# Optimization experiments

Hardware: AMD Instinct MI355X
Metric: run time of the kernel (lower is better)

The kernel has to match this reference:

```python
import jax, jax.numpy as jnp
import numpy as np

PD = 3                      # spatial feature dim (z, y, x)
HB = 1024                   # hash base per lattice coordinate
HOFF = 512                  # offset: lattice coords assumed in [-512, 511]
FILL = np.int32(2**31 - 1)  # sentinel for padded hash slots
EPS = 2.220446049250313e-16 # np.finfo('float').eps as in the torch module

def _elev_mat():
    # Embedding onto hyperplane sum(x)=0 with std-dev scale factors
    # (canonical permutohedral-lattice elevation, Adams et al.).
    E = np.zeros((PD + 1, PD), np.float32)
    E[0] = 1.0
    for i in range(1, PD + 1):
        E[i, i - 1] = -i
        E[i, i:] = 1.0
    inv_std = np.sqrt(2.0 / 3.0) * (PD + 1)
    scale = inv_std / np.sqrt(np.arange(1, PD + 1) * np.arange(2, PD + 2))
    return (E * scale[None, :]).astype(np.float32)

_EMAT = _elev_mat()
_IU = np.triu(np.ones((PD + 1, PD + 1), bool), 1)   # j > i
_IL = np.tril(np.ones((PD + 1, PD + 1), bool), -1)  # j < i

def _hash(k):  # (..., PD) int32 -> (...,) int32, injective for |coord| < 512
    return ((k[..., 0] + HOFF) * HB + (k[..., 1] + HOFF)) * HB + (k[..., 2] + HOFF)

def permutohedral(values, features):
    """Splat-blur-slice Gaussian filter. values (N,VD), features (N,PD)."""
    N, VD = values.shape
    elevated = features @ jnp.asarray(_EMAT).T                  # (N, PD+1)
    # nearest remainder-0 lattice point (nearest multiple of PD+1, ties -> down)
    v = elevated / (PD + 1)
    up, down = jnp.ceil(v), jnp.floor(v)
    rem0 = jnp.where(up - v < v - down, up, down) * (PD + 1)
    diff = elevated - rem0
    lt = diff[:, :, None] < diff[:, None, :]
    le = diff[:, :, None] <= diff[:, None, :]
    rank = (lt & _IU).sum(-1) + (le & _IL).sum(-1)              # (N, PD+1) int32
    rank = rank + jnp.round(rem0.sum(-1) / (PD + 1)).astype(rank.dtype)[:, None]
    shift = jnp.where(rank < 0, PD + 1, 0) + jnp.where(rank > PD, -(PD + 1), 0)
    rank = rank + shift
    rem0 = rem0 + shift.astype(rem0.dtype)
    # barycentric coordinates inside the enclosing simplex
    t = (elevated - rem0) / (PD + 1)                            # (N, PD+1)
    ohA = jax.nn.one_hot(PD - rank, PD + 2, dtype=values.dtype)
    ohB = jax.nn.one_hot(PD + 1 - rank, PD + 2, dtype=values.dtype)
    b = (ohA * t[..., None]).sum(1) - (ohB * t[..., None]).sum(1)
    b = b.at[:, 0].add(1.0 + b[:, PD + 1])
    bary = b[:, :PD + 1]                                        # (N, PD+1)
    # keys of the PD+1 simplex vertices (first PD coords; last is implied)
    rem0i = rem0[:, :PD].astype(jnp.int32)
    ranki = rank[:, :PD].astype(jnp.int32)
    r = jnp.arange(PD + 1, dtype=jnp.int32)[None, :, None]
    keys = rem0i[:, None, :] + jnp.where(ranki[:, None, :] >= PD + 1 - r, r - (PD + 1), r)  # (N,PD+1,PD)
    h = _hash(keys).reshape(-1)                                 # (N*(PD+1),)
    M = h.shape[0]
    uh, inv = jnp.unique(h, size=M, fill_value=FILL, return_inverse=True)
    inv = inv.reshape(-1)
    # splat
    contrib = (values[:, None, :] * bary[:, :, None]).reshape(M, VD)
    lat = jax.ops.segment_sum(contrib, inv, num_segments=M)     # (M, VD)
    # decode unique keys from the (invertible) hash
    k2 = uh % HB - HOFF
    tq = uh // HB
    k1 = tq % HB - HOFF
    k0 = tq // HB - HOFF
    ukeys = jnp.stack([k0, k1, k2], -1).astype(jnp.int32)       # (M, PD)
    valid = (uh != FILL)[:, None]
    # blur with [0.5, 1, 0.5] along each of the PD+1 lattice directions
    def lookup(nk, lat_):
        nh = _hash(nk)
        idx = jnp.clip(jnp.searchsorted(uh, nh), 0, M - 1)
        ok = (uh[idx] == nh)[:, None]
        return jnp.where(ok, lat_[idx], 0.0)
    for j in range(PD + 1):
        o = np.ones(PD, np.int32)
        if j < PD:
            o[j] = -PD
        o = jnp.asarray(o)
        lat = jnp.where(valid, lat + 0.5 * (lookup(ukeys + o, lat) + lookup(ukeys - o, lat)), 0.0)
    # slice
    alpha = 1.0 / (1.0 + 2.0 ** (-PD))
    return alpha * jnp.einsum('nr,nrv->nv', bary, lat[inv.reshape(-1, PD + 1)])

def spatial_features(image, v_gamma, sigma_gamma):
    _, d, h, w = image.shape
    z = jnp.arange(d, dtype=jnp.float32)[:, None, None]
    y = jnp.arange(h, dtype=jnp.float32)[None, :, None]
    x = jnp.arange(w, dtype=jnp.float32)[None, None, :]
    zz = v_gamma[0] * jnp.broadcast_to(z, (d, h, w)) / sigma_gamma[0]
    xx = v_gamma[1] * jnp.broadcast_to(x, (d, h, w)) / sigma_gamma[1]
    yy = v_gamma[2] * jnp.broadcast_to(y, (d, h, w)) / sigma_gamma[2]
    return jnp.stack([zz, yy, xx], axis=3)                      # (d,h,w,3)

def setup_inputs() -> dict:
    key = jax.random.key(0)
    k1, k2 = jax.random.split(key)
    C, D, H, W = 4, 64, 128, 128
    return {
        'input_': jax.random.normal(k1, (C, D, H, W), jnp.float32),
        'image': jax.random.normal(k2, (1, D, H, W), jnp.float32),
        'v_gamma': jnp.ones((3,), jnp.float32),       # nn.Parameter init [1,1,1]
        'sigma_gamma': 5.0 * jnp.ones((3,), jnp.float32),
    }

def reference(input_, image, v_gamma, sigma_gamma):
    C, d, h, w = input_.shape
    N = d * h * w
    feats = spatial_features(image, v_gamma, sigma_gamma).reshape(N, PD)
    # filter q and the all-ones normalizer in one pass (linear per channel)
    vals = jnp.concatenate([input_.reshape(C, N).T, jnp.ones((N, 1), jnp.float32)], axis=1)
    out = permutohedral(vals, feats)
    q = out[:, :C].T.reshape(C, d, h, w)
    norm = out[:, C].reshape(1, d, h, w)
    return q * (1.0 / (norm + EPS))
```

## Files before the change

kernel.cpp:

```cpp
#include <hip/hip_runtime.h>


#define DD    64
#define HHH   128
#define WWW   128
#define NPTS  (DD * HHH * WWW)
#define LATN  (1 << 17)
#define LATF  (LATN * 5)
#define NCPY  2
#define DQ    7
#define CELLS (DQ * DQ * DQ * 4)
#define MASKW ((CELLS + 31) / 32)
#define NOID  0x7fffffff

__device__ __forceinline__ int encK(int K0, int K1, int K2) {
    return ((K2 >> 2) << 12) | ((K1 >> 2) << 7) | ((K0 >> 2) << 2) | (K0 & 3);
}

__device__ __forceinline__ int pl_geom(int z, int y, int x,
                                       const float* __restrict__ vg,
                                       const float* __restrict__ sg,
                                       int* Kout , float* bout) {
    float f0 = vg[0] * (float)z / sg[0];
    float f1 = vg[2] * (float)y / sg[2];
    float f2 = vg[1] * (float)x / sg[1];

    const float m00 = (float)2.3094010767585034;
    const float m01 = (float)1.3333333333333333;
    const float m02 = (float)0.9428090415820634;
    const float m21 = (float)-2.6666666666666665;
    const float m32 = (float)-2.8284271247461903;

    float e[4];
    e[0] =  m00 * f0 + m01 * f1 + m02 * f2;
    e[1] = -m00 * f0 + m01 * f1 + m02 * f2;
    e[2] =  m21 * f1 + m02 * f2;
    e[3] =  m32 * f2;

    float rem0[4];
    int sumr = 0;
    #pragma unroll
    for (int i = 0; i < 4; ++i) {
        rem0[i] = rintf(e[i] * 0.25f) * 4.0f;
        sumr += (int)rem0[i];
    }
    sumr /= 4;

    float diff[4];
    #pragma unroll
    for (int i = 0; i < 4; ++i) diff[i] = e[i] - rem0[i];
    int rank[4] = {0, 0, 0, 0};
    #pragma unroll
    for (int i = 0; i < 4; ++i)
        #pragma unroll
        for (int j = i + 1; j < 4; ++j) {
            if (diff[i] < diff[j]) rank[i]++; else rank[j]++;
        }

    #pragma unroll
    for (int i = 0; i < 4; ++i) {
        rank[i] += sumr;
        if (rank[i] < 0)      { rank[i] += 4; rem0[i] += 4.0f; }
        else if (rank[i] > 3) { rank[i] -= 4; rem0[i] -= 4.0f; }
    }

    float b[5] = {0.f, 0.f, 0.f, 0.f, 0.f};
    #pragma unroll
    for (int i = 0; i < 4; ++i) {
        float t = (e[i] - rem0[i]) * 0.25f;
        b[3 - rank[i]] += t;
        b[4 - rank[i]] -= t;
    }
    b[0] += 1.0f + b[4];

    int k0 = (int)rem0[0] + 16, k1 = (int)rem0[1] + 48, k2 = (int)rem0[2] + 88;
    #pragma unroll
    for (int r = 0; r < 4; ++r) {
        int o0 = (rank[0] >= 4 - r) ? (r - 4) : r;
        int o1 = (rank[1] >= 4 - r) ? (r - 4) : r;
        int o2 = (rank[2] >= 4 - r) ? (r - 4) : r;
        Kout[r * 3 + 0] = k0 + o0;
        Kout[r * 3 + 1] = k1 + o1;
        Kout[r * 3 + 2] = k2 + o2;
        bout[r] = b[r];
    }
    return ((k0 >> 2) + 32) | (((k1 >> 2) + 32) << 7) | (((k2 >> 2) + 32) << 14) |
           (rank[0] << 21) | (rank[1] << 23) | (rank[2] << 25);
}

__device__ __forceinline__ void pl_claim(int key, unsigned int* __restrict__ exists,
                                         int* __restrict__ wcnt, int* __restrict__ wl) {
    if (atomicExch(&exists[key], 1u) == 0u) {
        int p = atomicAdd(wcnt, 1);
        wl[p] = key;
    }
}

__device__ __forceinline__ int make_id(const int* K, int B0, int B1, int B2) {
    int l0 = K[0] - B0, l1 = K[1] - B1, l2 = K[2] - B2;
    if (((unsigned)l0 < 4u * DQ) & ((unsigned)l1 < 4u * DQ) & ((unsigned)l2 < 4u * DQ))
        return ((((l2 >> 2) * DQ) + (l1 >> 2)) * DQ + (l0 >> 2)) * 4 + (l0 & 3);
    return ~encK(K[0] & 127, K[1] & 127, K[2] & 127);
}

__device__ __forceinline__ void pl_emit(int id, const float* a,
                                        float* sacc, unsigned int* smask,
                                        float* __restrict__ mycopy,
                                        unsigned int* __restrict__ exists,
                                        int* __restrict__ wcnt, int* __restrict__ wl) {
    if (id >= 0) {
        #pragma unroll
        for (int c = 0; c < 5; ++c) atomicAdd(&sacc[id * 5 + c], a[c]);
        atomicOr(&smask[id >> 5], 1u << (id & 31));
    } else {
        int key = ~id;
        float* L = mycopy + (size_t)key * 5;
        #pragma unroll
        for (int c = 0; c < 5; ++c) atomicAdd(L + c, a[c]);
        pl_claim(key, exists, wcnt, wl);
    }
}

__global__ __launch_bounds__(256, 4)
void pl_splat(const float* __restrict__ vals, const float* __restrict__ vg,
              const float* __restrict__ sg, float* __restrict__ latc,
              unsigned int* __restrict__ exists,
              int* __restrict__ wcnt, int* __restrict__ wl) {
    __shared__ float4 sacc4[CELLS * 5 / 4 + 1];
    __shared__ unsigned int smask[MASKW];
    float* sacc = (float*)sacc4;
    for (int i = threadIdx.x; i < CELLS * 5 / 4 + 1; i += 256)
        sacc4[i] = make_float4(0.f, 0.f, 0.f, 0.f);
    if (threadIdx.x < MASKW) smask[threadIdx.x] = 0u;
    __syncthreads();

    int bt = blockIdx.x;
    int tx = (bt & 3) << 5;
    int ty = ((bt >> 2) & 15) << 3;
    int tz = (bt >> 6) << 2;

    float s0 = vg[0] / sg[0], s1 = vg[2] / sg[2], s2 = vg[1] / sg[1];
    const float m00 = 2.30940104f, m01 = 1.33333325f, m02 = 0.942809045f,
                m21 = -2.66666651f;
    float A0z = m00 * s0, A0y = m01 * s1, A0x = m02 * s2;
    float A1z = -A0z,     A1y = A0y,      A1x = A0x;
    float A2y = m21 * s1, A2x = A0x;
    float e0o = A0z * tz + A0y * ty + A0x * tx;
    float e1o = A1z * tz + A1y * ty + A1x * tx;
    float e2o = A2y * ty + A2x * tx;
    float e0m = e0o + fminf(0.f, A0z) * 3 + fminf(0.f, A0y) * 7 + fminf(0.f, A0x) * 31;
    float e1m = e1o + fminf(0.f, A1z) * 3 + fminf(0.f, A1y) * 7 + fminf(0.f, A1x) * 31;
    float e2m = e2o + fminf(0.f, A2y) * 7 + fminf(0.f, A2x) * 31;
    int B0 = ((int)floorf(e0m + 16.f - 7.f)) & ~3;
    int B1 = ((int)floorf(e1m + 48.f - 7.f)) & ~3;
    int B2 = ((int)floorf(e2m + 88.f - 7.f)) & ~3;

    int xs = threadIdx.x & 7;
    int xsl = ((xs & 3) << 1) | (xs >> 2);
    int x0 = tx + (xsl << 2);
    int y  = ty + ((threadIdx.x >> 3) & 7);
    int z  = tz + (threadIdx.x >> 6);
    int n0 = (z << 14) + (y << 7) + x0;

    float4 q0 = *(const float4*)(vals + n0);
    float4 q1 = *(const float4*)(vals + NPTS + n0);
    float4 q2 = *(const float4*)(vals + 2 * NPTS + n0);
    float4 q3 = *(const float4*)(vals + 3 * NPTS + n0);
    float ch0[4] = {q0.x, q0.y, q0.z, q0.w};
    float ch1[4] = {q1.x, q1.y, q1.z, q1.w};
    float ch2[4] = {q2.x, q2.y, q2.z, q2.w};
    float ch3[4] = {q3.x, q3.y, q3.z, q3.w};

    float* mycopy = latc + (size_t)(blockIdx.x & (NCPY - 1)) * LATF;

    int cid[4], pid[4];
    float cacc[4][5], pacc[4][5];
    {
        int K[12]; float b[4];
        pl_geom(z, y, x0, vg, sg, K, b);
        #pragma unroll
        for (int r = 0; r < 4; ++r) {
            cid[r] = make_id(K + r * 3, B0, B1, B2);
            pid[r] = NOID;
            float w = b[r];
            cacc[r][0] = w * ch0[0]; cacc[r][1] = w * ch1[0];
            cacc[r][2] = w * ch2[0]; cacc[r][3] = w * ch3[0];
            cacc[r][4] = w;
        }
    }
    #pragma unroll
    for (int p = 1; p < 4; ++p) {
        int K[12]; float b[4];
        pl_geom(z, y, x0 + p, vg, sg, K, b);
        #pragma unroll
        for (int r = 0; r < 4; ++r) {
            int id = make_id(K + r * 3, B0, B1, B2);
            float w = b[r];
            if (id == cid[r]) {
                cacc[r][0] += w * ch0[p]; cacc[r][1] += w * ch1[p];
                cacc[r][2] += w * ch2[p]; cacc[r][3] += w * ch3[p];
                cacc[r][4] += w;
            } else {
                if (pid[r] != NOID)
                    pl_emit(pid[r], pacc[r], sacc, smask, mycopy, exists, wcnt, wl);
                pid[r] = cid[r];
                #pragma unroll
                for (int c = 0; c < 5; ++c) pacc[r][c] = cacc[r][c];
                cid[r] = id;
                cacc[r][0] = w * ch0[p]; cacc[r][1] = w * ch1[p];
                cacc[r][2] = w * ch2[p]; cacc[r][3] = w * ch3[p];
                cacc[r][4] = w;
            }
        }
    }
    #pragma unroll
    for (int r = 0; r < 4; ++r) {
        if (pid[r] != NOID)
            pl_emit(pid[r], pacc[r], sacc, smask, mycopy, exists, wcnt, wl);
        pl_emit(cid[r], cacc[r], sacc, smask, mycopy, exists, wcnt, wl);
    }
    __syncthreads();

    for (int i = threadIdx.x; i < CELLS; i += 256) {
        if (!((smask[i >> 5] >> (i & 31)) & 1u)) continue;
        int r = i & 3, q = i >> 2;
        int l0q = q % DQ; int t = q / DQ;
        int l1q = t % DQ; int l2q = t / DQ;
        int K0 = B0 + (l0q << 2) + r;
        int K1 = B1 + (l1q << 2) + r;
        int K2 = B2 + (l2q << 2) + r;
        int key = encK(K0 & 127, K1 & 127, K2 & 127);
        pl_claim(key, exists, wcnt, wl);
        float* L = mycopy + (size_t)key * 5;
        #pragma unroll
        for (int c = 0; c < 5; ++c) atomicAdd(L + c, sacc[i * 5 + c]);
    }
}

__global__ __launch_bounds__(256)
void pl_blur(const unsigned int* __restrict__ exists,
             const int* __restrict__ wl, const int* __restrict__ wcnt,
             const float* __restrict__ in, float* __restrict__ out,
             int d0, int d1, int d2, int first) {
    int total = (*wcnt) * 5;
    for (int i = blockIdx.x * 256 + threadIdx.x; i < total; i += 256 * 256) {
        int ci = i / 5, c = i - ci * 5;
        int didx = wl[ci];
        int r  = didx & 3;
        int K0 = (((didx >> 2)  & 31) << 2) | r;
        int K1 = (((didx >> 7)  & 31) << 2) | r;
        int K2 = (((didx >> 12) & 31) << 2) | r;
        size_t o = (size_t)didx * 5 + c;
        float ctr, n = 0.f;
        if (first) ctr = in[o] + in[LATF + o];
        else       ctr = in[o];
        #pragma unroll
        for (int sgn = 0; sgn < 2; ++sgn) {
            int P0 = K0 + (sgn ? -d0 : d0);
            int P1 = K1 + (sgn ? -d1 : d1);
            int P2 = K2 + (sgn ? -d2 : d2);
            if (((unsigned)P0 < 128u) & ((unsigned)P1 < 128u) & ((unsigned)P2 < 128u)) {
                int nk = encK(P0, P1, P2);
                if (exists[nk]) {
                    size_t no = (size_t)nk * 5 + c;
                    if (first) n += in[no] + in[LATF + no];
                    else       n += in[no];
                }
            }
        }
        out[o] = ctr + 0.5f * n;
    }
}

__global__ __launch_bounds__(256)
void pl_slice(const float* __restrict__ vg, const float* __restrict__ sg,
              const float* __restrict__ lat, float* __restrict__ out) {
    int t = blockIdx.x * 256 + threadIdx.x;
    int n0 = t << 2;
    int z = n0 >> 14;
    int y = (n0 >> 7) & 127;
    int x0 = n0 & 127;
    float r0[4], r1[4], r2[4], r3[4];
    int Sprev = -1;
    float Lv[4][5];
    #pragma unroll
    for (int p = 0; p < 4; ++p) {
        int K[12]; float b[4];
        int S = pl_geom(z, y, x0 + p, vg, sg, K, b);
        if (S != Sprev) {
            Sprev = S;
            #pragma unroll
            for (int r = 0; r < 4; ++r) {
                int key = encK(K[r * 3] & 127, K[r * 3 + 1] & 127, K[r * 3 + 2] & 127);
                const float* L = lat + (size_t)key * 5;
                #pragma unroll
                for (int c = 0; c < 5; ++c) Lv[r][c] = L[c];
            }
        }
        float a0 = 0.f, a1 = 0.f, a2 = 0.f, a3 = 0.f, a4 = 0.f;
        #pragma unroll
        for (int r = 0; r < 4; ++r) {
            float w = b[r];
            a0 += w * Lv[r][0]; a1 += w * Lv[r][1]; a2 += w * Lv[r][2];
            a3 += w * Lv[r][3]; a4 += w * Lv[r][4];
        }
        const float alpha = (float)(1.0 / 1.125);
        float invn = 1.0f / (alpha * a4 + (float)2.220446049250313e-16);
        r0[p] = alpha * a0 * invn;
        r1[p] = alpha * a1 * invn;
        r2[p] = alpha * a2 * invn;
        r3[p] = alpha * a3 * invn;
    }
    *(float4*)(out + n0)            = make_float4(r0[0], r0[1], r0[2], r0[3]);
    *(float4*)(out + NPTS + n0)     = make_float4(r1[0], r1[1], r1[2], r1[3]);
    *(float4*)(out + 2 * NPTS + n0) = make_float4(r2[0], r2[1], r2[2], r2[3]);
    *(float4*)(out + 3 * NPTS + n0) = make_float4(r3[0], r3[1], r3[2], r3[3]);
}

extern "C" void kernel_launch(void* const* d_in, const int* in_sizes, int n_in,
                              void* d_out, int out_size, void* d_ws, size_t ws_size,
                              hipStream_t stream) {
    const float* input = (const float*)d_in[0];
    const float* vg = (const float*)d_in[2];
    const float* sg = (const float*)d_in[3];
    float* out = (float*)d_out;

    char* ws = (char*)d_ws;
    float* latc = (float*)ws;
    unsigned int* exists = (unsigned int*)(latc + (size_t)NCPY * LATF);
    int* wcnt = (int*)(exists + LATN);
    int*   wl = (int*)(wcnt + 64);
    float* A  = (float*)(wl + LATN);
    float* B  = A + LATF;

    size_t zbytes = (size_t)NCPY * LATF * 4 + (size_t)LATN * 4 + 256;
    hipMemsetAsync(ws, 0, zbytes, stream);

    pl_splat<<<1024, dim3(256), 0, stream>>>(input, vg, sg, latc, exists, wcnt, wl);

    pl_blur<<<256, dim3(256), 0, stream>>>(exists, wl, wcnt, latc, A, -3, 1, 1, 1);
    pl_blur<<<256, dim3(256), 0, stream>>>(exists, wl, wcnt, A, B, 1, -3, 1, 0);
    pl_blur<<<256, dim3(256), 0, stream>>>(exists, wl, wcnt, B, A, 1, 1, -3, 0);
    pl_blur<<<256, dim3(256), 0, stream>>>(exists, wl, wcnt, A, B, 1, 1, 1, 0);

    pl_slice<<<NPTS / 4 / 256, dim3(256), 0, stream>>>(vg, sg, B, out);
}
```

Baseline: 154.0 us.

## Pad lattice to stride 8, enlarge splat tiles, simplify run-length emit

Lattice entries move from a stride of 5 floats to a stride of 8, so slice can read each vertex with one float4 load plus a scalar and rows stay aligned. The splat kernel now uses 512-thread blocks covering 8 z-slices, halving the block count so more points share each block's shared-memory accumulation. The per-thread pending/current double buffer is replaced by a single accumulator that emits on every cell change. The trade-offs are a larger lattice memset and more memory traffic in the blur passes, plus a possible shared-memory cell window overflow, since DQ stays at 7 while the z extent doubled (out-of-window cells fall back to global atomics).

Result: no change. 155.1 us (+0.7%).

```diff
diff --git a/kernel.cpp b/kernel.cpp
--- a/kernel.cpp
+++ b/kernel.cpp
@@ -6,12 +6,12 @@
 #define WWW   128
 #define NPTS  (DD * HHH * WWW)
 #define LATN  (1 << 17)
-#define LATF  (LATN * 5)
+#define LATSTR 8
+#define LATF  (LATN * LATSTR)
 #define NCPY  2
 #define DQ    7
 #define CELLS (DQ * DQ * DQ * 4)
 #define MASKW ((CELLS + 31) / 32)
-#define NOID  0x7fffffff
 
 __device__ __forceinline__ int encK(int K0, int K1, int K2) {
     return ((K2 >> 2) << 12) | ((K1 >> 2) << 7) | ((K0 >> 2) << 2) | (K0 & 3);
@@ -114,14 +114,14 @@
         atomicOr(&smask[id >> 5], 1u << (id & 31));
     } else {
         int key = ~id;
-        float* L = mycopy + (size_t)key * 5;
+        float* L = mycopy + (size_t)key * LATSTR;
         #pragma unroll
         for (int c = 0; c < 5; ++c) atomicAdd(L + c, a[c]);
         pl_claim(key, exists, wcnt, wl);
     }
 }
 
-__global__ __launch_bounds__(256, 4)
+__global__ __launch_bounds__(512, 4)
 void pl_splat(const float* __restrict__ vals, const float* __restrict__ vg,
               const float* __restrict__ sg, float* __restrict__ latc,
               unsigned int* __restrict__ exists,
@@ -129,7 +129,7 @@
     __shared__ float4 sacc4[CELLS * 5 / 4 + 1];
     __shared__ unsigned int smask[MASKW];
     float* sacc = (float*)sacc4;
-    for (int i = threadIdx.x; i < CELLS * 5 / 4 + 1; i += 256)
+    for (int i = threadIdx.x; i < CELLS * 5 / 4 + 1; i += 512)
         sacc4[i] = make_float4(0.f, 0.f, 0.f, 0.f);
     if (threadIdx.x < MASKW) smask[threadIdx.x] = 0u;
     __syncthreads();
@@ -137,7 +137,7 @@
     int bt = blockIdx.x;
     int tx = (bt & 3) << 5;
     int ty = ((bt >> 2) & 15) << 3;
-    int tz = (bt >> 6) << 2;
+    int tz = (bt >> 6) << 3;
 
     float s0 = vg[0] / sg[0], s1 = vg[2] / sg[2], s2 = vg[1] / sg[1];
     const float m00 = 2.30940104f, m01 = 1.33333325f, m02 = 0.942809045f,
@@ -148,8 +148,8 @@
     float e0o = A0z * tz + A0y * ty + A0x * tx;
     float e1o = A1z * tz + A1y * ty + A1x * tx;
     float e2o = A2y * ty + A2x * tx;
-    float e0m = e0o + fminf(0.f, A0z) * 3 + fminf(0.f, A0y) * 7 + fminf(0.f, A0x) * 31;
-    float e1m = e1o + fminf(0.f, A1z) * 3 + fminf(0.f, A1y) * 7 + fminf(0.f, A1x) * 31;
+    float e0m = e0o + fminf(0.f, A0z) * 7 + fminf(0.f, A0y) * 7 + fminf(0.f, A0x) * 31;
+    float e1m = e1o + fminf(0.f, A1z) * 7 + fminf(0.f, A1y) * 7 + fminf(0.f, A1x) * 31;
     float e2m = e2o + fminf(0.f, A2y) * 7 + fminf(0.f, A2x) * 31;
     int B0 = ((int)floorf(e0m + 16.f - 7.f)) & ~3;
     int B1 = ((int)floorf(e1m + 48.f - 7.f)) & ~3;
@@ -173,19 +173,18 @@
 
     float* mycopy = latc + (size_t)(blockIdx.x & (NCPY - 1)) * LATF;
 
-    int cid[4], pid[4];
-    float cacc[4][5], pacc[4][5];
+    int cid[4];
+    float acc[4][5];
     {
         int K[12]; float b[4];
         pl_geom(z, y, x0, vg, sg, K, b);
         #pragma unroll
         for (int r = 0; r < 4; ++r) {
             cid[r] = make_id(K + r * 3, B0, B1, B2);
-            pid[r] = NOID;
             float w = b[r];
-            cacc[r][0] = w * ch0[0]; cacc[r][1] = w * ch1[0];
-            cacc[r][2] = w * ch2[0]; cacc[r][3] = w * ch3[0];
-            cacc[r][4] = w;
+            acc[r][0] = w * ch0[0]; acc[r][1] = w * ch1[0];
+            acc[r][2] = w * ch2[0]; acc[r][3] = w * ch3[0];
+            acc[r][4] = w;
         }
     }
     #pragma unroll
@@ -197,31 +196,25 @@
             int id = make_id(K + r * 3, B0, B1, B2);
             float w = b[r];
             if (id == cid[r]) {
-                cacc[r][0] += w * ch0[p]; cacc[r][1] += w * ch1[p];
-                cacc[r][2] += w * ch2[p]; cacc[r][3] += w * ch3[p];
-                cacc[r][4] += w;
+                acc[r][0] += w * ch0[p]; acc[r][1] += w * ch1[p];
+                acc[r][2] += w * ch2[p]; acc[r][3] += w * ch3[p];
+                acc[r][4] += w;
             } else {
-                if (pid[r] != NOID)
-                    pl_emit(pid[r], pacc[r], sacc, smask, mycopy, exists, wcnt, wl);
-                pid[r] = cid[r];
-                #pragma unroll
-                for (int c = 0; c < 5; ++c) pacc[r][c] = cacc[r][c];
+                pl_emit(cid[r], acc[r], sacc, smask, mycopy, exists, wcnt, wl);
                 cid[r] = id;
-                cacc[r][0] = w * ch0[p]; cacc[r][1] = w * ch1[p];
-                cacc[r][2] = w * ch2[p]; cacc[r][3] = w * ch3[p];
-                cacc[r][4] = w;
+                acc[r][0] = w * ch0[p]; acc[r][1] = w * ch1[p];
+                acc[r][2] = w * ch2[p]; acc[r][3] = w * ch3[p];
+                acc[r][4] = w;
             }
         }
     }
     #pragma unroll
-    for (int r = 0; r < 4; ++r) {
-        if (pid[r] != NOID)
-            pl_emit(pid[r], pacc[r], sacc, smask, mycopy, exists, wcnt, wl);
-        pl_emit(cid[r], cacc[r], sacc, smask, mycopy, exists, wcnt, wl);
-    }
+    for (int r = 0; r < 4; ++r)
+        pl_emit(cid[r], acc[r], sacc, smask, mycopy, exists, wcnt, wl);
+
     __syncthreads();
 
-    for (int i = threadIdx.x; i < CELLS; i += 256) {
+    for (int i = threadIdx.x; i < CELLS; i += 512) {
         if (!((smask[i >> 5] >> (i & 31)) & 1u)) continue;
         int r = i & 3, q = i >> 2;
         int l0q = q % DQ; int t = q / DQ;
@@ -231,7 +224,7 @@
         int K2 = B2 + (l2q << 2) + r;
         int key = encK(K0 & 127, K1 & 127, K2 & 127);
         pl_claim(key, exists, wcnt, wl);
-        float* L = mycopy + (size_t)key * 5;
+        float* L = mycopy + (size_t)key * LATSTR;
         #pragma unroll
         for (int c = 0; c < 5; ++c) atomicAdd(L + c, sacc[i * 5 + c]);
     }
@@ -250,7 +243,7 @@
         int K0 = (((didx >> 2)  & 31) << 2) | r;
         int K1 = (((didx >> 7)  & 31) << 2) | r;
         int K2 = (((didx >> 12) & 31) << 2) | r;
-        size_t o = (size_t)didx * 5 + c;
+        size_t o = (size_t)didx * LATSTR + c;
         float ctr, n = 0.f;
         if (first) ctr = in[o] + in[LATF + o];
         else       ctr = in[o];
@@ -262,7 +255,7 @@
             if (((unsigned)P0 < 128u) & ((unsigned)P1 < 128u) & ((unsigned)P2 < 128u)) {
                 int nk = encK(P0, P1, P2);
                 if (exists[nk]) {
-                    size_t no = (size_t)nk * 5 + c;
+                    size_t no = (size_t)nk * LATSTR + c;
                     if (first) n += in[no] + in[LATF + no];
                     else       n += in[no];
                 }
@@ -282,7 +275,8 @@
     int x0 = n0 & 127;
     float r0[4], r1[4], r2[4], r3[4];
     int Sprev = -1;
-    float Lv[4][5];
+    float4 Lv4[4];
+    float  Lv1[4];
     #pragma unroll
     for (int p = 0; p < 4; ++p) {
         int K[12]; float b[4];
@@ -292,17 +286,17 @@
             #pragma unroll
             for (int r = 0; r < 4; ++r) {
                 int key = encK(K[r * 3] & 127, K[r * 3 + 1] & 127, K[r * 3 + 2] & 127);
-                const float* L = lat + (size_t)key * 5;
-                #pragma unroll
-                for (int c = 0; c < 5; ++c) Lv[r][c] = L[c];
+                const float* L = lat + (size_t)key * LATSTR;
+                Lv4[r] = *(const float4*)L;
+                Lv1[r] = L[4];
             }
         }
         float a0 = 0.f, a1 = 0.f, a2 = 0.f, a3 = 0.f, a4 = 0.f;
         #pragma unroll
         for (int r = 0; r < 4; ++r) {
             float w = b[r];
-            a0 += w * Lv[r][0]; a1 += w * Lv[r][1]; a2 += w * Lv[r][2];
-            a3 += w * Lv[r][3]; a4 += w * Lv[r][4];
+            a0 += w * Lv4[r].x; a1 += w * Lv4[r].y; a2 += w * Lv4[r].z;
+            a3 += w * Lv4[r].w; a4 += w * Lv1[r];
         }
         const float alpha = (float)(1.0 / 1.125);
         float invn = 1.0f / (alpha * a4 + (float)2.220446049250313e-16);
@@ -336,7 +330,7 @@
     size_t zbytes = (size_t)NCPY * LATF * 4 + (size_t)LATN * 4 + 256;
     hipMemsetAsync(ws, 0, zbytes, stream);
 
-    pl_splat<<<1024, dim3(256), 0, stream>>>(input, vg, sg, latc, exists, wcnt, wl);
+    pl_splat<<<512, dim3(512), 0, stream>>>(input, vg, sg, latc, exists, wcnt, wl);
 
     pl_blur<<<256, dim3(256), 0, stream>>>(exists, wl, wcnt, latc, A, -3, 1, 1, 1);
     pl_blur<<<256, dim3(256), 0, stream>>>(exists, wl, wcnt, A, B, 1, -3, 1, 0);
```
